# Optimization experiments

Hardware: AMD Instinct MI355X
Metric: run time of the kernel (lower is better)

The kernel has to match this reference:

```python
import jax, jax.numpy as jnp
import numpy as np

B, N = 65536, 24
THRESHOLD = 0.5
EXCLUDED_POINTS = [0]
EXCLUDED_PAIRS = [(2, 3)]


def _static_mask():
    # exclusion mask (excluded points / pairs) AND no-self-pair mask; [N, N]
    m = np.ones((N, N), dtype=bool)
    for p in EXCLUDED_POINTS:
        if p < N:
            m[p, :] = False
            m[:, p] = False
    for a, b in EXCLUDED_PAIRS:
        if a < N and b < N:
            m[a, b] = False
            m[b, a] = False
    np.fill_diagonal(m, False)
    return jnp.asarray(m)


def setup_inputs() -> dict:
    key = jax.random.key(0)
    pos = jax.random.normal(key, (B, N, 3), dtype=jnp.float32)
    return {"pos": pos}


def reference(pos):
    mask = _static_mask()  # [N, N] static
    diff = pos[:, :, None, :] - pos[:, None, :, :]  # [B, N, N, 3]
    sq = jnp.sum(diff * diff, axis=-1)              # [B, N, N]
    # safe sqrt: masked-out entries (incl. diagonal zeros) get a dummy value
    dist = jnp.sqrt(jnp.where(mask, sq, 1.0))
    collision = (dist < THRESHOLD) & mask           # [B, N, N] bool
    w = collision.astype(pos.dtype)
    nd = dist / THRESHOLD
    exp_losses = jnp.exp(-(nd * nd))
    num = jnp.sum(w)
    total = jnp.where(num > 0, jnp.sum(exp_losses * w) / jnp.maximum(num, 1.0), 0.0)
    return total + 1e-6
```

## Files before the change

### kernel.cpp

```cpp
#include <hip/hip_runtime.h>


#define NPTS 24
#define BLK 128
#define BATCHES_PER_BLK 64
#define LDS_STRIDE 73

__global__ __launch_bounds__(BLK)
void collision_main(const float* __restrict__ pos, float2* __restrict__ ws) {
    __shared__ float lds[BATCHES_PER_BLK * LDS_STRIDE];
    const int t = threadIdx.x;
    const int blockBase = blockIdx.x * BATCHES_PER_BLK;

    const float4* gp = (const float4*)pos + (size_t)blockBase * 18;
    #pragma unroll
    for (int k = 0; k < 9; ++k) {
        int f4 = t + k * BLK;
        float4 v = gp[f4];
        int b  = f4 / 18;
        int e4 = f4 % 18;
        float* dst = &lds[b * LDS_STRIDE + e4 * 4];
        dst[0] = v.x; dst[1] = v.y; dst[2] = v.z; dst[3] = v.w;
    }
    __syncthreads();

    float px[NPTS], py[NPTS], pz[NPTS];
    const float* src = &lds[(t & 63) * LDS_STRIDE];
    #pragma unroll
    for (int i = 0; i < NPTS; ++i) {
        px[i] = src[3 * i + 0];
        py[i] = src[3 * i + 1];
        pz[i] = src[3 * i + 2];
    }

    float s = 0.0f;
    int   cc = 0;
    auto acc = [&](int i, int j) {
        float dx = px[i] - px[j];
        float dy = py[i] - py[j];
        float dz = pz[i] - pz[j];
        float sq = fmaf(dx, dx, fmaf(dy, dy, dz * dz));
        bool  w  = sq < 0.25f;
        cc += (int)__popcll(__ballot(w));
        float e  = __expf(-4.0f * sq);
        s += w ? e : 0.0f;
    };
    if (t < 64) {
        #pragma unroll
        for (int i = 1; i <= 6; ++i)
            #pragma unroll
            for (int j = i + 1; j < NPTS; ++j) {
                if (i == 2 && j == 3) continue;
                acc(i, j);
            }
        #pragma unroll
        for (int j = 8; j < 18; ++j) acc(7, j);
    } else {
        #pragma unroll
        for (int j = 18; j < NPTS; ++j) acc(7, j);
        #pragma unroll
        for (int i = 8; i < NPTS; ++i)
            #pragma unroll
            for (int j = i + 1; j < NPTS; ++j) acc(i, j);
    }

    #pragma unroll
    for (int off = 32; off >= 1; off >>= 1)
        s += __shfl_down(s, off, 64);

    __shared__ float sred[2];
    __shared__ int   cred[2];
    const int wv = t >> 6;
    if ((t & 63) == 0) { sred[wv] = s; cred[wv] = cc; }
    __syncthreads();
    if (t == 0) {
        float2 p;
        p.x = sred[0] + sred[1];
        p.y = (float)(cred[0] + cred[1]);
        ws[blockIdx.x] = p;
    }
}

__global__ __launch_bounds__(256)
void collision_reduce(const float* __restrict__ ws, float* __restrict__ out) {
    const float4* p4 = (const float4*)ws;
    const int t = threadIdx.x;
    float s = 0.0f, c = 0.0f;
    #pragma unroll
    for (int k = 0; k < 2; ++k) {
        float4 v = p4[t + k * 256];
        s += v.x + v.z;
        c += v.y + v.w;
    }
    #pragma unroll
    for (int off = 32; off >= 1; off >>= 1) {
        s += __shfl_down(s, off, 64);
        c += __shfl_down(c, off, 64);
    }
    __shared__ float sb[4], cb[4];
    if ((t & 63) == 0) { sb[t >> 6] = s; cb[t >> 6] = c; }
    __syncthreads();
    if (t == 0) {
        s = sb[0] + sb[1] + sb[2] + sb[3];
        c = cb[0] + cb[1] + cb[2] + cb[3];
        float total = (c > 0.0f) ? (s / fmaxf(c, 1.0f)) : 0.0f;
        out[0] = total + 1e-6f;
    }
}

extern "C" void kernel_launch(void* const* d_in, const int* in_sizes, int n_in,
                              void* d_out, int out_size, void* d_ws, size_t ws_size,
                              hipStream_t stream) {
    const float* pos = (const float*)d_in[0];
    float* out = (float*)d_out;
    float2* ws = (float2*)d_ws;

    const int B = in_sizes[0] / (NPTS * 3);
    const int nblocks = B / BATCHES_PER_BLK;

    collision_main<<<nblocks, BLK, 0, stream>>>(pos, ws);
    collision_reduce<<<1, 256, 0, stream>>>((const float*)ws, out);
}
```

Before: 70.08 us.

## Split pair work across four waves with packed v2f math and exp2

```diff
diff --git a/kernel.cpp b/kernel.cpp
--- a/kernel.cpp
+++ b/kernel.cpp
@@ -2,11 +2,60 @@
 
 
 #define NPTS 24
-#define BLK 128
+#define BLK 256
 #define BATCHES_PER_BLK 64
 #define LDS_STRIDE 73
 
-__global__ __launch_bounds__(BLK)
+typedef float v2f __attribute__((ext_vector_type(2)));
+
+struct Pts {
+    v2f x[12], y[12], z[12];
+};
+
+#define EXP2_SCALE (-5.770780163555852f)
+
+template<int I>
+__device__ __forceinline__ void row(const Pts& p, v2f& acc, int& cc) {
+    constexpr int JS = (I == 2) ? 4 : (I + 1);
+    constexpr int H = I >> 1;
+    constexpr int L = I & 1;
+    const float xi = L ? p.x[H].y : p.x[H].x;
+    const float yi = L ? p.y[H].y : p.y[H].x;
+    const float zi = L ? p.z[H].y : p.z[H].x;
+
+    if constexpr (JS & 1) {
+        constexpr int JH = JS >> 1;
+        float dx = xi - p.x[JH].y;
+        float dy = yi - p.y[JH].y;
+        float dz = zi - p.z[JH].y;
+        float sq = fmaf(dx, dx, fmaf(dy, dy, dz * dz));
+        bool  w  = sq < 0.25f;
+        cc += (int)__popcll(__ballot(w));
+        float e = __builtin_amdgcn_exp2f(sq * EXP2_SCALE);
+        acc.x += w ? e : 0.0f;
+    }
+
+    constexpr int G0 = (JS + 1) >> 1;
+    const v2f xiv = {xi, xi}, yiv = {yi, yi}, ziv = {zi, zi};
+    #pragma unroll
+    for (int g = G0; g < 12; ++g) {
+        v2f dx = xiv - p.x[g];
+        v2f dy = yiv - p.y[g];
+        v2f dz = ziv - p.z[g];
+        v2f sq = __builtin_elementwise_fma(dx, dx,
+                 __builtin_elementwise_fma(dy, dy, dz * dz));
+        v2f m  = sq * (v2f){EXP2_SCALE, EXP2_SCALE};
+        bool w0 = sq.x < 0.25f;
+        bool w1 = sq.y < 0.25f;
+        cc += (int)__popcll(__ballot(w0));
+        cc += (int)__popcll(__ballot(w1));
+        float e0 = __builtin_amdgcn_exp2f(m.x);
+        float e1 = __builtin_amdgcn_exp2f(m.y);
+        acc += (v2f){ w0 ? e0 : 0.0f, w1 ? e1 : 0.0f };
+    }
+}
+
+__global__ __launch_bounds__(BLK, 4)
 void collision_main(const float* __restrict__ pos, float2* __restrict__ ws) {
     __shared__ float lds[BATCHES_PER_BLK * LDS_STRIDE];
     const int t = threadIdx.x;
@@ -14,70 +63,58 @@
 
     const float4* gp = (const float4*)pos + (size_t)blockBase * 18;
     #pragma unroll
-    for (int k = 0; k < 9; ++k) {
+    for (int k = 0; k < 5; ++k) {
         int f4 = t + k * BLK;
-        float4 v = gp[f4];
-        int b  = f4 / 18;
-        int e4 = f4 % 18;
-        float* dst = &lds[b * LDS_STRIDE + e4 * 4];
-        dst[0] = v.x; dst[1] = v.y; dst[2] = v.z; dst[3] = v.w;
+        if (f4 < 1152) {
+            float4 v = gp[f4];
+            int b  = f4 / 18;
+            int e4 = f4 % 18;
+            float* dst = &lds[b * LDS_STRIDE + e4 * 4];
+            dst[0] = v.x; dst[1] = v.y; dst[2] = v.z; dst[3] = v.w;
+        }
     }
     __syncthreads();
 
-    float px[NPTS], py[NPTS], pz[NPTS];
+    Pts p;
     const float* src = &lds[(t & 63) * LDS_STRIDE];
     #pragma unroll
-    for (int i = 0; i < NPTS; ++i) {
-        px[i] = src[3 * i + 0];
-        py[i] = src[3 * i + 1];
-        pz[i] = src[3 * i + 2];
+    for (int g = 0; g < 12; ++g) {
+        p.x[g] = (v2f){src[6 * g + 0], src[6 * g + 3]};
+        p.y[g] = (v2f){src[6 * g + 1], src[6 * g + 4]};
+        p.z[g] = (v2f){src[6 * g + 2], src[6 * g + 5]};
     }
 
-    float s = 0.0f;
-    int   cc = 0;
-    auto acc = [&](int i, int j) {
-        float dx = px[i] - px[j];
-        float dy = py[i] - py[j];
-        float dz = pz[i] - pz[j];
-        float sq = fmaf(dx, dx, fmaf(dy, dy, dz * dz));
-        bool  w  = sq < 0.25f;
-        cc += (int)__popcll(__ballot(w));
-        float e  = __expf(-4.0f * sq);
-        s += w ? e : 0.0f;
-    };
-    if (t < 64) {
-        #pragma unroll
-        for (int i = 1; i <= 6; ++i)
-            #pragma unroll
-            for (int j = i + 1; j < NPTS; ++j) {
-                if (i == 2 && j == 3) continue;
-                acc(i, j);
-            }
-        #pragma unroll
-        for (int j = 8; j < 18; ++j) acc(7, j);
+    v2f acc = {0.0f, 0.0f};
+    int cc = 0;
+    const int q = t >> 6;
+    if (q == 0) {
+        row< 1>(p, acc, cc); row< 8>(p, acc, cc); row<10>(p, acc, cc);
+        row<15>(p, acc, cc); row<18>(p, acc, cc);
+    } else if (q == 1) {
+        row< 2>(p, acc, cc); row< 6>(p, acc, cc); row<11>(p, acc, cc);
+        row<14>(p, acc, cc); row<19>(p, acc, cc); row<22>(p, acc, cc);
+    } else if (q == 2) {
+        row< 3>(p, acc, cc); row< 7>(p, acc, cc); row< 9>(p, acc, cc);
+        row<16>(p, acc, cc); row<17>(p, acc, cc);
     } else {
-        #pragma unroll
-        for (int j = 18; j < NPTS; ++j) acc(7, j);
-        #pragma unroll
-        for (int i = 8; i < NPTS; ++i)
-            #pragma unroll
-            for (int j = i + 1; j < NPTS; ++j) acc(i, j);
+        row< 4>(p, acc, cc); row< 5>(p, acc, cc); row<12>(p, acc, cc);
+        row<13>(p, acc, cc); row<20>(p, acc, cc); row<21>(p, acc, cc);
     }
 
+    float s = acc.x + acc.y;
     #pragma unroll
     for (int off = 32; off >= 1; off >>= 1)
         s += __shfl_down(s, off, 64);
 
-    __shared__ float sred[2];
-    __shared__ int   cred[2];
-    const int wv = t >> 6;
-    if ((t & 63) == 0) { sred[wv] = s; cred[wv] = cc; }
+    __shared__ float sred[4];
+    __shared__ int   cred[4];
+    if ((t & 63) == 0) { sred[q] = s; cred[q] = cc; }
     __syncthreads();
     if (t == 0) {
-        float2 p;
-        p.x = sred[0] + sred[1];
-        p.y = (float)(cred[0] + cred[1]);
-        ws[blockIdx.x] = p;
+        float2 pr;
+        pr.x = sred[0] + sred[1] + sred[2] + sred[3];
+        pr.y = (float)(cred[0] + cred[1] + cred[2] + cred[3]);
+        ws[blockIdx.x] = pr;
     }
 }
 
```

After: 72.15 us. 3.0% more time.
